# Kernel tuning notes

Measured on AMD Instinct MI355X. Metric: run time of the kernel, lower is better.

## Reference

```python
import jax, jax.numpy as jnp
import numpy as np
import math

CH_IN, MID, PS, DSTATE = 64, 128, 1024, 16
DTRANK = math.ceil(PS / 16)  # 64
B, H, W = 4, 256, 256


def conv2d(x, w, b=None, stride=1, pad=0, groups=1):
    out = jax.lax.conv_general_dilated(
        x, w, (stride, stride), [(pad, pad), (pad, pad)],
        feature_group_count=groups, dimension_numbers=('NCHW', 'OIHW', 'NCHW'))
    return out if b is None else out + b[None, :, None, None]


def groupnorm(x, g, b, ngroups=2, eps=1e-5):
    bb, c, hh, ww = x.shape
    xr = x.reshape(bb, ngroups, c // ngroups, hh, ww)
    mu = xr.mean(axis=(2, 3, 4), keepdims=True)
    var = xr.var(axis=(2, 3, 4), keepdims=True)
    xn = ((xr - mu) * jax.lax.rsqrt(var + eps)).reshape(bb, c, hh, ww)
    return xn * g[None, :, None, None] + b[None, :, None, None]


def silu(x):
    return x * jax.nn.sigmoid(x)


def selective_scan(u, delta, A, Bm, Cm, D):
    # u, delta: (b, l, d); A: (d, n); Bm, Cm: (b, l, n); D: (d,)
    dA = jnp.exp(jnp.einsum('bld,dn->bldn', delta, A))          # (b,l,d,n)
    dBu = (delta * u)[..., None] * Bm[:, :, None, :]             # (b,l,d,n)
    bsz, l, d = u.shape
    n = A.shape[1]

    def step(carry, inp):
        dA_i, dBu_i, C_i = inp                                   # (b,d,n),(b,d,n),(b,n)
        carry = dA_i * carry + dBu_i
        y = jnp.einsum('bdn,bn->bd', carry, C_i)
        return carry, y

    x0 = jnp.zeros((bsz, d, n), dtype=u.dtype)
    _, ys = jax.lax.scan(step, x0, (dA.transpose(1, 0, 2, 3), dBu.transpose(1, 0, 2, 3), Cm.transpose(1, 0, 2)))
    y = ys.transpose(1, 0, 2)                                    # (b,l,d)
    return y + u * D


def mamba_block(x, inproj_w, conv_w, conv_b, xproj_w, dtp_w, dtp_b, alog, dd):
    xr = conv2d(x, inproj_w, None, 1, 1, MID // 2)               # (b, 2*MID, h, w)
    xs, res = jnp.split(xr, 2, axis=1)
    xs = silu(conv2d(xs, conv_w, conv_b, 1, 0, MID // 2))
    b, c, h, w = xs.shape
    u = xs.reshape(b, c, h * w)                                  # (b, l=c, d=h*w)
    A = -jnp.exp(alog.astype(jnp.float32))                       # (d, n)
    x_dbl = jnp.einsum('bld,kd->blk', u, xproj_w)
    delta, Bm, Cm = jnp.split(x_dbl, [DTRANK, DTRANK + DSTATE], axis=-1)
    delta = jax.nn.softplus(jnp.einsum('blr,dr->bld', delta, dtp_w) + dtp_b)
    y = selective_scan(u, delta, A, Bm, Cm, dd.astype(jnp.float32))
    y = y.reshape(b, c, h, w)
    return y * silu(res)


def forward(x, w_in, b_in,
            gn0_g, gn0_b, inproj0_w, conv0_w, conv0_b, xproj0_w, dtp0_w, dtp0_b, alog0, dd0,
            gn1_g, gn1_b, inproj1_w, conv1_w, conv1_b, xproj1_w, dtp1_w, dtp1_b, alog1, dd1,
            w_out, b_out):
    h = conv2d(x, w_in, b_in, 8, 0, CH_IN // 2)                  # (B, MID, H/8, W/8)
    h = mamba_block(groupnorm(h, gn0_g, gn0_b), inproj0_w, conv0_w, conv0_b, xproj0_w, dtp0_w, dtp0_b, alog0, dd0) + h
    h = mamba_block(groupnorm(h, gn1_g, gn1_b), inproj1_w, conv1_w, conv1_b, xproj1_w, dtp1_w, dtp1_b, alog1, dd1) + h
    out = conv2d(h, w_out, b_out, 1, 0, CH_IN // 2)
    out = jax.image.resize(out, (out.shape[0], out.shape[1], out.shape[2] * 8, out.shape[3] * 8), method='bilinear')
    return out


def setup_inputs():
    key = jax.random.key(0)
    ks = jax.random.split(key, 16)
    def rn(k, shp, s=0.05):
        return s * jax.random.normal(k, shp, jnp.float32)
    alog = jnp.log(jnp.broadcast_to(jnp.arange(1, DSTATE + 1, dtype=jnp.float32), (PS, DSTATE)))
    inp = {
        'x': jax.random.normal(ks[0], (B, CH_IN, H, W), jnp.float32),
        'w_in': rn(ks[1], (MID, 2, 8, 8)), 'b_in': jnp.zeros((MID,), jnp.float32),
        'gn0_g': jnp.ones((MID,), jnp.float32), 'gn0_b': jnp.zeros((MID,), jnp.float32),
        'inproj0_w': rn(ks[2], (2 * MID, 2, 3, 3)),
        'conv0_w': rn(ks[3], (MID, 2, 1, 1)), 'conv0_b': jnp.zeros((MID,), jnp.float32),
        'xproj0_w': rn(ks[4], (DTRANK + 2 * DSTATE, PS), 0.02),
        'dtp0_w': rn(ks[5], (PS, DTRANK), 0.02), 'dtp0_b': rn(ks[6], (PS,), 0.02),
        'alog0': alog, 'dd0': jnp.ones((PS,), jnp.float32),
        'gn1_g': jnp.ones((MID,), jnp.float32), 'gn1_b': jnp.zeros((MID,), jnp.float32),
        'inproj1_w': rn(ks[7], (2 * MID, 2, 3, 3)),
        'conv1_w': rn(ks[8], (MID, 2, 1, 1)), 'conv1_b': jnp.zeros((MID,), jnp.float32),
        'xproj1_w': rn(ks[9], (DTRANK + 2 * DSTATE, PS), 0.02),
        'dtp1_w': rn(ks[10], (PS, DTRANK), 0.02), 'dtp1_b': rn(ks[11], (PS,), 0.02),
        'alog1': alog, 'dd1': jnp.ones((PS,), jnp.float32),
        'w_out': rn(ks[12], (MID, MID // (CH_IN // 2), 1, 1)), 'b_out': jnp.zeros((MID,), jnp.float32),
    }
    return inp


def reference(x, w_in, b_in,
              gn0_g, gn0_b, inproj0_w, conv0_w, conv0_b, xproj0_w, dtp0_w, dtp0_b, alog0, dd0,
              gn1_g, gn1_b, inproj1_w, conv1_w, conv1_b, xproj1_w, dtp1_w, dtp1_b, alog1, dd1,
              w_out, b_out):
    return forward(x, w_in, b_in,
                   gn0_g, gn0_b, inproj0_w, conv0_w, conv0_b, xproj0_w, dtp0_w, dtp0_b, alog0, dd0,
                   gn1_g, gn1_b, inproj1_w, conv1_w, conv1_b, xproj1_w, dtp1_w, dtp1_b, alog1, dd1,
                   w_out, b_out)
```

## Files before the change

kernel.cpp:

```cpp
#include <hip/hip_runtime.h>
#include <hip/hip_bf16.h>

#define BN 4
#define MID 128
#define P 1024
#define PS 1024
#define DSTATE 16
#define DTRANK 64
#define XD 96
#define HOUT 256

typedef __hip_bfloat16 bf16;

__device__ __forceinline__ float b2f(bf16 v) { return __bfloat162float(v); }
__device__ __forceinline__ float dload(const void* p, int i, bool isbf) {
  return isbf ? b2f(((const bf16*)p)[i]) : ((const float*)p)[i];
}
__device__ __forceinline__ float bfl(unsigned u) {
  union { unsigned i; float f; } c; c.i = u << 16; return c.f;
}
__device__ __forceinline__ float bfh(unsigned u) {
  union { unsigned i; float f; } c; c.i = u & 0xffff0000u; return c.f;
}

#define NPARAM 24
#define TOTAL_PARAMS 392192
#define CONV_PER_BLOCK 766
struct PtrPack { const void* p[NPARAM]; };

__device__ __forceinline__ void find_tensor(int dst, int& tt, int& off) {
  const int offs[NPARAM + 1] = {0,16384,16512,16640,16768,21376,21632,21760,120064,185600,
                                186624,203008,204032,204160,204288,208896,209152,209280,
                                307584,373120,374144,390528,391552,392064,392192};
  int t = 0, base = 0;
#pragma unroll
  for (int q = 1; q < NPARAM; ++q) {
    if (dst >= offs[q]) { t = q; base = offs[q]; }
  }
  tt = t; off = dst - base;
}

__global__ __launch_bounds__(256) void conv_in_kernel(
    const void* __restrict__ x, const unsigned* __restrict__ alog_raw,
    PtrPack pk, float* __restrict__ pp, float* __restrict__ h,
    float2* __restrict__ partA) {
  bool isbf = (alog_raw[0] != 0u);
  int blk = blockIdx.x, t = threadIdx.x;

  for (int i = t; i < CONV_PER_BLOCK; i += 256) {
    int dst = blk * CONV_PER_BLOCK + i;
    int tt, off;
    find_tensor(dst, tt, off);
    int src = off;
    if (tt == 7 || tt == 17) {
      int j = off & 3, q = off >> 2;
      int k = q % 96, d4 = q / 96;
      src = k * 1024 + d4 * 4 + j;
    } else if (tt == 8 || tt == 18) {
      src = (off & 1023) * 64 + (off >> 10);
    }
    pp[dst] = dload(pk.p[tt], src, isbf);
  }

  __shared__ float wlds[512];
  __shared__ float blds[4];
  __shared__ float ls[8];
  int tid = blk * 256 + t;
  int p = tid & 1023; int g = (tid >> 10) & 31; int b = tid >> 15;
  for (int q = t; q < 512; q += 256) {
    int i = q >> 8, kh = (q >> 5) & 7, j = (q >> 3) & 3, kw = q & 7;
    wlds[q] = dload(pk.p[0], (g * 4 + j) * 128 + i * 64 + kh * 8 + kw, isbf);
  }
  if (t < 4) blds[t] = dload(pk.p[1], g * 4 + t, isbf);
  __syncthreads();

  int oy = p >> 5, ox = p & 31;
  float acc0 = blds[0], acc1 = blds[1], acc2 = blds[2], acc3 = blds[3];
  if (isbf) {
    const uint4* xp = (const uint4*)x;
    size_t base = ((size_t)b * 64 + g * 2) * 8192;
    for (int i = 0; i < 2; ++i) {
      size_t cb = base + (size_t)i * 8192 + (size_t)oy * 256 + ox;
#pragma unroll
      for (int kh = 0; kh < 8; ++kh) {
        uint4 v = xp[cb + kh * 32];
        float xv[8] = {bfl(v.x),bfh(v.x),bfl(v.y),bfh(v.y),bfl(v.z),bfh(v.z),bfl(v.w),bfh(v.w)};
        const float* wk = &wlds[(i * 8 + kh) * 32];
#pragma unroll
        for (int kw = 0; kw < 8; ++kw) {
          float xvv = xv[kw];
          acc0 += xvv * wk[kw];
          acc1 += xvv * wk[8 + kw];
          acc2 += xvv * wk[16 + kw];
          acc3 += xvv * wk[24 + kw];
        }
      }
    }
  } else {
    const float4* xf = (const float4*)x;
    size_t base = ((size_t)b * 64 + g * 2) * 16384;
    for (int i = 0; i < 2; ++i) {
      size_t cb = base + (size_t)i * 16384 + (size_t)oy * 512 + ox * 2;
#pragma unroll
      for (int kh = 0; kh < 8; ++kh) {
        float4 v0 = xf[cb + kh * 64];
        float4 v1 = xf[cb + kh * 64 + 1];
        float xv[8] = {v0.x,v0.y,v0.z,v0.w,v1.x,v1.y,v1.z,v1.w};
        const float* wk = &wlds[(i * 8 + kh) * 32];
#pragma unroll
        for (int kw = 0; kw < 8; ++kw) {
          float xvv = xv[kw];
          acc0 += xvv * wk[kw];
          acc1 += xvv * wk[8 + kw];
          acc2 += xvv * wk[16 + kw];
          acc3 += xvv * wk[24 + kw];
        }
      }
    }
  }
  size_t ob = ((size_t)b * 128 + g * 4) * 1024 + p;
  h[ob] = acc0; h[ob + 1024] = acc1; h[ob + 2048] = acc2; h[ob + 3072] = acc3;

  float s  = acc0 + acc1 + acc2 + acc3;
  float s2 = acc0*acc0 + acc1*acc1 + acc2*acc2 + acc3*acc3;
#pragma unroll
  for (int off = 32; off > 0; off >>= 1) { s += __shfl_xor(s, off); s2 += __shfl_xor(s2, off); }
  int wid = t >> 6;
  if ((t & 63) == 0) { ls[wid * 2] = s; ls[wid * 2 + 1] = s2; }
  __syncthreads();
  if (t == 0)
    partA[blk] = make_float2(ls[0] + ls[2] + ls[4] + ls[6], ls[1] + ls[3] + ls[5] + ls[7]);
}

__global__ __launch_bounds__(256) void fused_u_kernel(
    const float* __restrict__ h, const float2* __restrict__ partial, int perB, int cnt,
    const float* __restrict__ gng, const float* __restrict__ gnb,
    const float* __restrict__ iw, const float* __restrict__ cw,
    const float* __restrict__ cb, float* __restrict__ u) {
  int blk = blockIdx.x;
  int h2 = blk & 1, g3 = (blk >> 1) & 31, b = blk >> 6;
  int ic0 = g3 * 2;
  __shared__ float tile[2][34][36];
  __shared__ float sred[2];
  if (threadIdx.x < 64) {
    float s = 0.f, s2 = 0.f;
    int base = b * perB;
    for (int i = threadIdx.x; i < cnt; i += 64) { float2 v = partial[base + i]; s += v.x; s2 += v.y; }
#pragma unroll
    for (int off = 32; off > 0; off >>= 1) { s += __shfl_xor(s, off); s2 += __shfl_xor(s2, off); }
    if (threadIdx.x == 0) { sred[0] = s; sred[1] = s2; }
  }
  for (int t = threadIdx.x; t < 2448; t += 256) ((float*)tile)[t] = 0.f;
  __syncthreads();
  float mu = sred[0] * (1.f / 65536.f);
  float var = sred[1] * (1.f / 65536.f) - mu * mu;
  float rs = rsqrtf(var + 1e-5f);
  float a0 = rs * gng[ic0],     o0 = gnb[ic0]     - mu * a0;
  float a1 = rs * gng[ic0 + 1], o1 = gnb[ic0 + 1] - mu * a1;
  const float* h0 = h + ((size_t)b * MID + ic0) * P;
  for (int t = threadIdx.x; t < 2048; t += 256) {
    int ch = t >> 10, px = t & 1023, y = px >> 5, xx = px & 31;
    float v = h0[ch * P + px];
    tile[ch][y + 1][xx + 1] = ch ? (v * a1 + o1) : (v * a0 + o0);
  }
  __syncthreads();
  const float* w0 = iw + (size_t)(4 * g3) * 18;
#pragma unroll
  for (int q = 0; q < 2; ++q) {
    int px = h2 * 512 + q * 256 + threadIdx.x;
    int y = px >> 5, xx = px & 31;
    float nb0[9], nb1[9];
#pragma unroll
    for (int ky = 0; ky < 3; ++ky)
#pragma unroll
      for (int kx = 0; kx < 3; ++kx) {
        nb0[ky * 3 + kx] = tile[0][y + ky][xx + kx];
        nb1[ky * 3 + kx] = tile[1][y + ky][xx + kx];
      }
    float xsv[4];
#pragma unroll
    for (int s4 = 0; s4 < 4; ++s4) {
      const float* wr = w0 + s4 * 18;
      float acc = 0.f;
#pragma unroll
      for (int k = 0; k < 9; ++k) acc += nb0[k] * wr[k] + nb1[k] * wr[9 + k];
      xsv[s4] = acc;
    }
#pragma unroll
    for (int j = 0; j < 4; ++j) {
      int c = 4 * g3 + j;
      int e4 = (j >> 1) * 2;
      float acc = cb[c] + cw[2 * c] * xsv[e4] + cw[2 * c + 1] * xsv[e4 + 1];
      u[((size_t)b * MID + c) * P + px] = acc / (1.f + __expf(-acc));
    }
  }
}

__global__ __launch_bounds__(256) void xdbl_delta_kernel(
    const float* __restrict__ u, const float* __restrict__ xwp,
    const float* __restrict__ dwt, const float* __restrict__ db,
    float* __restrict__ dlt_t, float* __restrict__ u_t, float* __restrict__ bct) {
  int bl = blockIdx.x;
  int b = bl >> 7, l = bl & 127;
  int t = threadIdx.x;
  __shared__ float4 us[256];
  __shared__ float4 accs[96];
  __shared__ float xds[64];
  const float4* up = (const float4*)(u + (size_t)bl * P);
  us[t] = up[t];
  __syncthreads();

  float4 acc = make_float4(0.f, 0.f, 0.f, 0.f);
  if (t < 192) {
    int s = (t >= 96) ? 1 : 0, k = t - s * 96;
    const float4* wp = (const float4*)xwp;
#pragma unroll 4
    for (int i = 0; i < 128; ++i) {
      int d4 = 2 * i + s;
      float4 w4 = wp[d4 * 96 + k];
      float4 u4 = us[d4];
      acc.x += u4.x * w4.x; acc.y += u4.y * w4.y; acc.z += u4.z * w4.z; acc.w += u4.w * w4.w;
    }
    if (s) accs[k] = acc;
  } else {
    float* ubase = u_t + ((size_t)b * 1024) * 128 + l;
    const float* usf = (const float*)us;
    for (int i = t - 192; i < 1024; i += 64) ubase[(size_t)i * 128] = usf[i];
  }
  __syncthreads();
  if (t < 96) {
    float4 o = accs[t];
    acc.x += o.x; acc.y += o.y; acc.z += o.z; acc.w += o.w;
    float v = (acc.x + acc.y) + (acc.z + acc.w);
    if (t < 64) xds[t] = v;
    else bct[((size_t)b * 32 + (t - 64)) * 128 + l] = v;
  }
  __syncthreads();

  float a0 = db[t], a1 = db[t + 256], a2 = db[t + 512], a3 = db[t + 768];
#pragma unroll 8
  for (int r = 0; r < 64; ++r) {
    float xr = xds[r];
    const float* wr = dwt + r * 1024 + t;
    a0 += xr * wr[0];
    a1 += xr * wr[256];
    a2 += xr * wr[512];
    a3 += xr * wr[768];
  }
  float* dbase = dlt_t + ((size_t)b * 1024) * 128 + l;
  float vals[4] = {a0, a1, a2, a3};
#pragma unroll
  for (int j = 0; j < 4; ++j) {
    float a = vals[j];
    float sp = fmaxf(a, 0.f) + log1pf(__expf(-fabsf(a)));
    dbase[(size_t)(t + 256 * j) * 128] = sp;
  }
}

__global__ __launch_bounds__(256) void scan_kernel(
    const float* __restrict__ u_t, const float* __restrict__ dlt_t,
    const float* __restrict__ bct, const float* __restrict__ alog,
    const float* __restrict__ dd, float* __restrict__ y_t) {
  int tid = blockIdx.x * 256 + threadIdx.x;
  int n = tid & 15; int d = (tid >> 4) & 1023; int b = tid >> 14;
  float A = -__expf(alog[d * DSTATE + n]);
  float D = dd[d];
  const float4* ut = (const float4*)(u_t   + ((size_t)b * 1024 + d) * 128);
  const float4* dt = (const float4*)(dlt_t + ((size_t)b * 1024 + d) * 128);
  const float4* Bt = (const float4*)(bct + ((size_t)b * 32 + n) * 128);
  const float4* Ct = (const float4*)(bct + ((size_t)b * 32 + 16 + n) * 128);
  float4* yp = (float4*)(y_t + ((size_t)b * 1024 + d) * 128);
  float state = 0.f;
#pragma unroll 2
  for (int lc = 0; lc < 32; ++lc) {
    float4 dl4 = dt[lc], u4 = ut[lc], B4 = Bt[lc], C4 = Ct[lc];
    float4 yo;
#define SSTEP(c) { float dA = __expf(dl4.c * A); state = dA * state + dl4.c * u4.c * B4.c; \
    float yv = state * C4.c; yv += __shfl_xor(yv, 1, 16); yv += __shfl_xor(yv, 2, 16); \
    yv += __shfl_xor(yv, 4, 16); yv += __shfl_xor(yv, 8, 16); yo.c = yv + u4.c * D; }
    SSTEP(x) SSTEP(y) SSTEP(z) SSTEP(w)
#undef SSTEP
    if (n == 0) yp[lc] = yo;
  }
}

__global__ __launch_bounds__(256) void merge_res_kernel(
    const float* __restrict__ hin, const float2* __restrict__ partial, int perB, int cnt,
    const float* __restrict__ gng, const float* __restrict__ gnb,
    const float* __restrict__ iw, const float* __restrict__ y_t,
    float* __restrict__ hout, float2* __restrict__ part_out) {
  int blk = blockIdx.x;
  int h2 = blk & 1, gq = (blk >> 1) & 31, b = blk >> 6;
  int g = 32 + gq;
  int ic0 = g * 2;
  __shared__ float tile[2][34][36];
  __shared__ float sred[2];
  __shared__ float ls[8];
  if (threadIdx.x < 64) {
    float s = 0.f, s2 = 0.f;
    int base = b * perB + cnt;
    for (int i = threadIdx.x; i < cnt; i += 64) { float2 v = partial[base + i]; s += v.x; s2 += v.y; }
#pragma unroll
    for (int off = 32; off > 0; off >>= 1) { s += __shfl_xor(s, off); s2 += __shfl_xor(s2, off); }
    if (threadIdx.x == 0) { sred[0] = s; sred[1] = s2; }
  }
  for (int t = threadIdx.x; t < 2448; t += 256) ((float*)tile)[t] = 0.f;
  __syncthreads();
  float mu = sred[0] * (1.f / 65536.f);
  float var = sred[1] * (1.f / 65536.f) - mu * mu;
  float rs = rsqrtf(var + 1e-5f);
  float a0 = rs * gng[ic0],     o0 = gnb[ic0]     - mu * a0;
  float a1 = rs * gng[ic0 + 1], o1 = gnb[ic0 + 1] - mu * a1;
  const float* h0 = hin + ((size_t)b * MID + ic0) * P;
  for (int t = threadIdx.x; t < 2048; t += 256) {
    int ch = t >> 10, px = t & 1023, y = px >> 5, xx = px & 31;
    float v = h0[ch * P + px];
    tile[ch][y + 1][xx + 1] = ch ? (v * a1 + o1) : (v * a0 + o0);
  }
  __syncthreads();
  const float* w0 = iw + (size_t)(4 * g) * 18;
  float sacc = 0.f, s2acc = 0.f;
#pragma unroll
  for (int q = 0; q < 2; ++q) {
    int px = h2 * 512 + q * 256 + threadIdx.x;
    int y = px >> 5, xx = px & 31;
    float nb0[9], nb1[9];
#pragma unroll
    for (int ky = 0; ky < 3; ++ky)
#pragma unroll
      for (int kx = 0; kx < 3; ++kx) {
        nb0[ky * 3 + kx] = tile[0][y + ky][xx + kx];
        nb1[ky * 3 + kx] = tile[1][y + ky][xx + kx];
      }
    float4 yv4 = *(const float4*)(y_t + ((size_t)b * 1024 + px) * 128 + gq * 4);
    float yv[4] = {yv4.x, yv4.y, yv4.z, yv4.w};
#pragma unroll
    for (int j = 0; j < 4; ++j) {
      const float* wr = w0 + j * 18;
      float res = 0.f;
#pragma unroll
      for (int k = 0; k < 9; ++k) res += nb0[k] * wr[k] + nb1[k] * wr[9 + k];
      int c = 4 * gq + j;
      size_t oi = ((size_t)b * MID + c) * P + px;
      float s = res / (1.f + __expf(-res));
      float val = yv[j] * s + hin[oi];
      hout[oi] = val;
      sacc += val; s2acc += val * val;
    }
  }
  if (part_out) {
#pragma unroll
    for (int off = 32; off > 0; off >>= 1) { sacc += __shfl_xor(sacc, off); s2acc += __shfl_xor(s2acc, off); }
    int wid = threadIdx.x >> 6;
    if ((threadIdx.x & 63) == 0) { ls[wid * 2] = sacc; ls[wid * 2 + 1] = s2acc; }
    __syncthreads();
    if (threadIdx.x == 0)
      part_out[blk] = make_float2(ls[0] + ls[2] + ls[4] + ls[6], ls[1] + ls[3] + ls[5] + ls[7]);
  }
}

__global__ __launch_bounds__(256) void out_kernel(
    const float* __restrict__ h, const float* __restrict__ w, const float* __restrict__ bias,
    const unsigned* __restrict__ alog_raw, void* __restrict__ out) {
  int bc = blockIdx.x;
  int c = bc & 127, b = bc >> 7;
  int t = threadIdx.x;
  __shared__ float cop[1024];
  __shared__ float txs[256];
  __shared__ int x0s[256], x1s[256];
  {
    float cx = ((float)t + 0.5f) * 0.125f - 0.5f;
    int ix0 = (int)floorf(cx);
    txs[t] = cx - (float)ix0;
    x0s[t] = max(ix0, 0);
    x1s[t] = min(ix0 + 1, 31);
  }
  const float* hp = h + ((size_t)b * MID + (c & ~3)) * P;
  float w0 = w[c * 4], w1 = w[c * 4 + 1], w2 = w[c * 4 + 2], w3 = w[c * 4 + 3];
  float bo = bias[c];
  {
    const float4* h4 = (const float4*)hp;
    float4 v0 = h4[t], v1 = h4[256 + t], v2 = h4[512 + t], v3 = h4[768 + t];
    float4 a;
    a.x = bo + w0 * v0.x + w1 * v1.x + w2 * v2.x + w3 * v3.x;
    a.y = bo + w0 * v0.y + w1 * v1.y + w2 * v2.y + w3 * v3.y;
    a.z = bo + w0 * v0.z + w1 * v1.z + w2 * v2.z + w3 * v3.z;
    a.w = bo + w0 * v0.w + w1 * v1.w + w2 * v2.w + w3 * v3.w;
    ((float4*)cop)[t] = a;
  }
  __syncthreads();
  bool isbf = (alog_raw[0] != 0u);
  size_t obase = (size_t)bc * 16384;
  for (int gidx = t; gidx < 16384; gidx += 256) {
    int ox4 = gidx & 63, oy = gidx >> 6;
    float ty = txs[oy]; int y0 = x0s[oy], y1 = x1s[oy];
    const float* r0 = cop + y0 * 32;
    const float* r1 = cop + y1 * 32;
    float v[4];
#pragma unroll
    for (int j = 0; j < 4; ++j) {
      int ox = ox4 * 4 + j;
      float tx = txs[ox]; int xx0 = x0s[ox], xx1 = x1s[ox];
      float v00 = r0[xx0], v01 = r0[xx1], v10 = r1[xx0], v11 = r1[xx1];
      v[j] = (1.f - ty) * ((1.f - tx) * v00 + tx * v01) + ty * ((1.f - tx) * v10 + tx * v11);
    }
    if (isbf) {
      ushort4 s;
      s.x = __hip_bfloat16_raw(__float2bfloat16(v[0])).x;
      s.y = __hip_bfloat16_raw(__float2bfloat16(v[1])).x;
      s.z = __hip_bfloat16_raw(__float2bfloat16(v[2])).x;
      s.w = __hip_bfloat16_raw(__float2bfloat16(v[3])).x;
      ((ushort4*)out)[obase + gidx] = s;
    } else {
      ((float4*)out)[obase + gidx] = make_float4(v[0], v[1], v[2], v[3]);
    }
  }
}

extern "C" void kernel_launch(void* const* d_in, const int* in_sizes, int n_in,
                              void* d_out, int out_size, void* d_ws, size_t ws_size,
                              hipStream_t stream) {
  const void* x = d_in[0];
  const unsigned* alog_raw = (const unsigned*)d_in[11];

  PtrPack pk;
  for (int i = 0; i < NPARAM; ++i) pk.p[i] = d_in[i + 1];

  float* ws = (float*)d_ws;
  float* pp    = ws;
  float* h0    = pp + TOTAL_PARAMS;
  float* h1    = h0 + 524288;
  float* u     = h1 + 524288;
  float* u_t   = u + 524288;
  float* dlt_t = u_t + 524288;
  float* y_t   = dlt_t + 524288;
  float* bct   = y_t + 524288;
  float* partA = bct + 16384;
  float* partB = partA + 1024;

  const float* w_out = pp + 391552;
  const float* b_out = pp + 392064;
  const float* gn_g[2], *gn_b[2], *inproj_w[2], *conv_w[2], *conv_b[2],
             *xproj_w[2], *dtp_w[2], *dtp_b[2], *alog_f[2], *dd_f[2];
  for (int k = 0; k < 2; ++k) {
    const float* base = pp + 16512 + (size_t)k * 187520;
    gn_g[k] = base + 0;       gn_b[k] = base + 128;
    inproj_w[k] = base + 256; conv_w[k] = base + 4864;
    conv_b[k] = base + 5120;  xproj_w[k] = base + 5248;
    dtp_w[k] = base + 103552; dtp_b[k] = base + 169088;
    alog_f[k] = base + 170112; dd_f[k] = base + 186496;
  }

  conv_in_kernel<<<512, 256, 0, stream>>>(x, alog_raw, pk, pp, h0, (float2*)partA);

  float* hbuf[2] = { h0, h1 };
  const float2* partIn = (const float2*)partA;
  int perB = 128, cnt = 64;
  for (int blk = 0; blk < 2; ++blk) {
    float* hin  = hbuf[blk & 1];
    float* hout = hbuf[(blk + 1) & 1];
    fused_u_kernel<<<256, 256, 0, stream>>>(hin, partIn, perB, cnt, gn_g[blk], gn_b[blk],
                                            inproj_w[blk], conv_w[blk], conv_b[blk], u);
    xdbl_delta_kernel<<<512, 256, 0, stream>>>(u, xproj_w[blk], dtp_w[blk], dtp_b[blk],
                                               dlt_t, u_t, bct);
    scan_kernel<<<256, 256, 0, stream>>>(u_t, dlt_t, bct, alog_f[blk], dd_f[blk], y_t);
    merge_res_kernel<<<256, 256, 0, stream>>>(hin, partIn, perB, cnt, gn_g[blk], gn_b[blk],
                                              inproj_w[blk], y_t, hout,
                                              blk == 0 ? (float2*)partB : nullptr);
    partIn = (const float2*)partB; perB = 64; cnt = 32;
  }

  out_kernel<<<512, 256, 0, stream>>>(h0, w_out, b_out, alog_raw, d_out);
}
```

Measured before the change: 355.6 us.

## Fuse all stages into one persistent kernel with atomic grid barriers

Replaces the nine separate kernel launches with a single persistent kernel of 512 blocks that runs every stage and separates them with software grid barriers built on atomic counters, which are zeroed by a memset before launch. Fused_u and merge now use 512 blocks handling 256 pixels each instead of 256 blocks handling 512, and the scan stage idles half the blocks. The goal is to remove launch gaps and tail effects between stages. In exchange it depends on all 512 blocks being co-resident, since the barrier wait gives up after a bounded spin, and it adds barrier spin overhead and possible occupancy limits from the shared-memory union.

```diff
diff --git a/kernel.cpp b/kernel.cpp
--- a/kernel.cpp
+++ b/kernel.cpp
@@ -26,7 +26,30 @@
 #define NPARAM 24
 #define TOTAL_PARAMS 392192
 #define CONV_PER_BLOCK 766
+#define NBLK 512u
 struct PtrPack { const void* p[NPARAM]; };
+
+__device__ __forceinline__ void gsync(unsigned* slot) {
+  __syncthreads();
+  if (threadIdx.x == 0) {
+    __threadfence();
+    __hip_atomic_fetch_add(slot, 1u, __ATOMIC_RELAXED, __HIP_MEMORY_SCOPE_AGENT);
+    unsigned guard = 0;
+    while (__hip_atomic_load(slot, __ATOMIC_RELAXED, __HIP_MEMORY_SCOPE_AGENT) < NBLK) {
+      __builtin_amdgcn_s_sleep(2);
+      if (++guard > (1u << 24)) break;
+    }
+    __threadfence();
+  }
+  __syncthreads();
+}
+
+union Smem {
+  struct { float wlds[512]; float blds[4]; float ls[8]; } s0;
+  struct { float tile[2][34][36]; float sred[2]; float ls[8]; } s1;
+  struct { float4 us[256]; float4 accs[96]; float xds[64]; } s2;
+  struct { float cop[1024]; float txs[256]; int x0s[256]; int x1s[256]; } s5;
+};
 
 __device__ __forceinline__ void find_tensor(int dst, int& tt, int& off) {
   const int offs[NPARAM + 1] = {0,16384,16512,16640,16768,21376,21632,21760,120064,185600,
@@ -40,11 +63,9 @@
   tt = t; off = dst - base;
 }
 
-__global__ __launch_bounds__(256) void conv_in_kernel(
-    const void* __restrict__ x, const unsigned* __restrict__ alog_raw,
-    PtrPack pk, float* __restrict__ pp, float* __restrict__ h,
-    float2* __restrict__ partA) {
-  bool isbf = (alog_raw[0] != 0u);
+__device__ __forceinline__ void stage_conv_in(const void* __restrict__ x, bool isbf,
+    const PtrPack& pk, float* __restrict__ pp, float* __restrict__ h,
+    float2* __restrict__ partA, Smem& sm) {
   int blk = blockIdx.x, t = threadIdx.x;
 
   for (int i = t; i < CONV_PER_BLOCK; i += 256) {
@@ -62,20 +83,17 @@
     pp[dst] = dload(pk.p[tt], src, isbf);
   }
 
-  __shared__ float wlds[512];
-  __shared__ float blds[4];
-  __shared__ float ls[8];
   int tid = blk * 256 + t;
   int p = tid & 1023; int g = (tid >> 10) & 31; int b = tid >> 15;
   for (int q = t; q < 512; q += 256) {
     int i = q >> 8, kh = (q >> 5) & 7, j = (q >> 3) & 3, kw = q & 7;
-    wlds[q] = dload(pk.p[0], (g * 4 + j) * 128 + i * 64 + kh * 8 + kw, isbf);
-  }
-  if (t < 4) blds[t] = dload(pk.p[1], g * 4 + t, isbf);
+    sm.s0.wlds[q] = dload(pk.p[0], (g * 4 + j) * 128 + i * 64 + kh * 8 + kw, isbf);
+  }
+  if (t < 4) sm.s0.blds[t] = dload(pk.p[1], g * 4 + t, isbf);
   __syncthreads();
 
   int oy = p >> 5, ox = p & 31;
-  float acc0 = blds[0], acc1 = blds[1], acc2 = blds[2], acc3 = blds[3];
+  float acc0 = sm.s0.blds[0], acc1 = sm.s0.blds[1], acc2 = sm.s0.blds[2], acc3 = sm.s0.blds[3];
   if (isbf) {
     const uint4* xp = (const uint4*)x;
     size_t base = ((size_t)b * 64 + g * 2) * 8192;
@@ -85,7 +103,7 @@
       for (int kh = 0; kh < 8; ++kh) {
         uint4 v = xp[cb + kh * 32];
         float xv[8] = {bfl(v.x),bfh(v.x),bfl(v.y),bfh(v.y),bfl(v.z),bfh(v.z),bfl(v.w),bfh(v.w)};
-        const float* wk = &wlds[(i * 8 + kh) * 32];
+        const float* wk = &sm.s0.wlds[(i * 8 + kh) * 32];
 #pragma unroll
         for (int kw = 0; kw < 8; ++kw) {
           float xvv = xv[kw];
@@ -106,7 +124,7 @@
         float4 v0 = xf[cb + kh * 64];
         float4 v1 = xf[cb + kh * 64 + 1];
         float xv[8] = {v0.x,v0.y,v0.z,v0.w,v1.x,v1.y,v1.z,v1.w};
-        const float* wk = &wlds[(i * 8 + kh) * 32];
+        const float* wk = &sm.s0.wlds[(i * 8 + kh) * 32];
 #pragma unroll
         for (int kw = 0; kw < 8; ++kw) {
           float xvv = xv[kw];
@@ -126,34 +144,32 @@
 #pragma unroll
   for (int off = 32; off > 0; off >>= 1) { s += __shfl_xor(s, off); s2 += __shfl_xor(s2, off); }
   int wid = t >> 6;
-  if ((t & 63) == 0) { ls[wid * 2] = s; ls[wid * 2 + 1] = s2; }
+  if ((t & 63) == 0) { sm.s0.ls[wid * 2] = s; sm.s0.ls[wid * 2 + 1] = s2; }
   __syncthreads();
   if (t == 0)
-    partA[blk] = make_float2(ls[0] + ls[2] + ls[4] + ls[6], ls[1] + ls[3] + ls[5] + ls[7]);
-}
-
-__global__ __launch_bounds__(256) void fused_u_kernel(
-    const float* __restrict__ h, const float2* __restrict__ partial, int perB, int cnt,
-    const float* __restrict__ gng, const float* __restrict__ gnb,
-    const float* __restrict__ iw, const float* __restrict__ cw,
-    const float* __restrict__ cb, float* __restrict__ u) {
-  int blk = blockIdx.x;
-  int h2 = blk & 1, g3 = (blk >> 1) & 31, b = blk >> 6;
+    partA[blk] = make_float2(sm.s0.ls[0] + sm.s0.ls[2] + sm.s0.ls[4] + sm.s0.ls[6],
+                             sm.s0.ls[1] + sm.s0.ls[3] + sm.s0.ls[5] + sm.s0.ls[7]);
+}
+
+__device__ __forceinline__ void stage_fused_u(const float* __restrict__ h,
+    const float2* __restrict__ partial, const float* __restrict__ gng,
+    const float* __restrict__ gnb, const float* __restrict__ iw,
+    const float* __restrict__ cw, const float* __restrict__ cb,
+    float* __restrict__ u, Smem& sm) {
+  int pb = blockIdx.x;
+  int h4 = pb & 3, g3 = (pb >> 2) & 31, b = pb >> 7;
   int ic0 = g3 * 2;
-  __shared__ float tile[2][34][36];
-  __shared__ float sred[2];
   if (threadIdx.x < 64) {
-    float s = 0.f, s2 = 0.f;
-    int base = b * perB;
-    for (int i = threadIdx.x; i < cnt; i += 64) { float2 v = partial[base + i]; s += v.x; s2 += v.y; }
+    float2 v = partial[b * 128 + threadIdx.x];
+    float s = v.x, s2 = v.y;
 #pragma unroll
     for (int off = 32; off > 0; off >>= 1) { s += __shfl_xor(s, off); s2 += __shfl_xor(s2, off); }
-    if (threadIdx.x == 0) { sred[0] = s; sred[1] = s2; }
-  }
-  for (int t = threadIdx.x; t < 2448; t += 256) ((float*)tile)[t] = 0.f;
-  __syncthreads();
-  float mu = sred[0] * (1.f / 65536.f);
-  float var = sred[1] * (1.f / 65536.f) - mu * mu;
+    if (threadIdx.x == 0) { sm.s1.sred[0] = s; sm.s1.sred[1] = s2; }
+  }
+  for (int t = threadIdx.x; t < 2448; t += 256) ((float*)sm.s1.tile)[t] = 0.f;
+  __syncthreads();
+  float mu = sm.s1.sred[0] * (1.f / 65536.f);
+  float var = sm.s1.sred[1] * (1.f / 65536.f) - mu * mu;
   float rs = rsqrtf(var + 1e-5f);
   float a0 = rs * gng[ic0],     o0 = gnb[ic0]     - mu * a0;
   float a1 = rs * gng[ic0 + 1], o1 = gnb[ic0 + 1] - mu * a1;
@@ -161,53 +177,47 @@
   for (int t = threadIdx.x; t < 2048; t += 256) {
     int ch = t >> 10, px = t & 1023, y = px >> 5, xx = px & 31;
     float v = h0[ch * P + px];
-    tile[ch][y + 1][xx + 1] = ch ? (v * a1 + o1) : (v * a0 + o0);
+    sm.s1.tile[ch][y + 1][xx + 1] = ch ? (v * a1 + o1) : (v * a0 + o0);
   }
   __syncthreads();
   const float* w0 = iw + (size_t)(4 * g3) * 18;
-#pragma unroll
-  for (int q = 0; q < 2; ++q) {
-    int px = h2 * 512 + q * 256 + threadIdx.x;
-    int y = px >> 5, xx = px & 31;
-    float nb0[9], nb1[9];
-#pragma unroll
-    for (int ky = 0; ky < 3; ++ky)
-#pragma unroll
-      for (int kx = 0; kx < 3; ++kx) {
-        nb0[ky * 3 + kx] = tile[0][y + ky][xx + kx];
-        nb1[ky * 3 + kx] = tile[1][y + ky][xx + kx];
-      }
-    float xsv[4];
-#pragma unroll
-    for (int s4 = 0; s4 < 4; ++s4) {
-      const float* wr = w0 + s4 * 18;
-      float acc = 0.f;
-#pragma unroll
-      for (int k = 0; k < 9; ++k) acc += nb0[k] * wr[k] + nb1[k] * wr[9 + k];
-      xsv[s4] = acc;
-    }
-#pragma unroll
-    for (int j = 0; j < 4; ++j) {
-      int c = 4 * g3 + j;
-      int e4 = (j >> 1) * 2;
-      float acc = cb[c] + cw[2 * c] * xsv[e4] + cw[2 * c + 1] * xsv[e4 + 1];
-      u[((size_t)b * MID + c) * P + px] = acc / (1.f + __expf(-acc));
-    }
-  }
-}
-
-__global__ __launch_bounds__(256) void xdbl_delta_kernel(
-    const float* __restrict__ u, const float* __restrict__ xwp,
-    const float* __restrict__ dwt, const float* __restrict__ db,
-    float* __restrict__ dlt_t, float* __restrict__ u_t, float* __restrict__ bct) {
+  int px = h4 * 256 + threadIdx.x;
+  int y = px >> 5, xx = px & 31;
+  float nb0[9], nb1[9];
+#pragma unroll
+  for (int ky = 0; ky < 3; ++ky)
+#pragma unroll
+    for (int kx = 0; kx < 3; ++kx) {
+      nb0[ky * 3 + kx] = sm.s1.tile[0][y + ky][xx + kx];
+      nb1[ky * 3 + kx] = sm.s1.tile[1][y + ky][xx + kx];
+    }
+  float xsv[4];
+#pragma unroll
+  for (int s4 = 0; s4 < 4; ++s4) {
+    const float* wr = w0 + s4 * 18;
+    float acc = 0.f;
+#pragma unroll
+    for (int k = 0; k < 9; ++k) acc += nb0[k] * wr[k] + nb1[k] * wr[9 + k];
+    xsv[s4] = acc;
+  }
+#pragma unroll
+  for (int j = 0; j < 4; ++j) {
+    int c = 4 * g3 + j;
+    int e4 = (j >> 1) * 2;
+    float acc = cb[c] + cw[2 * c] * xsv[e4] + cw[2 * c + 1] * xsv[e4 + 1];
+    u[((size_t)b * MID + c) * P + px] = acc / (1.f + __expf(-acc));
+  }
+}
+
+__device__ __forceinline__ void stage_xdbl(const float* __restrict__ u,
+    const float* __restrict__ xwp, const float* __restrict__ dwt,
+    const float* __restrict__ db, float* __restrict__ dlt_t,
+    float* __restrict__ u_t, float* __restrict__ bct, Smem& sm) {
   int bl = blockIdx.x;
   int b = bl >> 7, l = bl & 127;
   int t = threadIdx.x;
-  __shared__ float4 us[256];
-  __shared__ float4 accs[96];
-  __shared__ float xds[64];
   const float4* up = (const float4*)(u + (size_t)bl * P);
-  us[t] = up[t];
+  sm.s2.us[t] = up[t];
   __syncthreads();
 
   float4 acc = make_float4(0.f, 0.f, 0.f, 0.f);
@@ -218,21 +228,21 @@
     for (int i = 0; i < 128; ++i) {
       int d4 = 2 * i + s;
       float4 w4 = wp[d4 * 96 + k];
-      float4 u4 = us[d4];
+      float4 u4 = sm.s2.us[d4];
       acc.x += u4.x * w4.x; acc.y += u4.y * w4.y; acc.z += u4.z * w4.z; acc.w += u4.w * w4.w;
     }
-    if (s) accs[k] = acc;
+    if (s) sm.s2.accs[k] = acc;
   } else {
     float* ubase = u_t + ((size_t)b * 1024) * 128 + l;
-    const float* usf = (const float*)us;
+    const float* usf = (const float*)sm.s2.us;
     for (int i = t - 192; i < 1024; i += 64) ubase[(size_t)i * 128] = usf[i];
   }
   __syncthreads();
   if (t < 96) {
-    float4 o = accs[t];
+    float4 o = sm.s2.accs[t];
     acc.x += o.x; acc.y += o.y; acc.z += o.z; acc.w += o.w;
     float v = (acc.x + acc.y) + (acc.z + acc.w);
-    if (t < 64) xds[t] = v;
+    if (t < 64) sm.s2.xds[t] = v;
     else bct[((size_t)b * 32 + (t - 64)) * 128 + l] = v;
   }
   __syncthreads();
@@ -240,7 +250,7 @@
   float a0 = db[t], a1 = db[t + 256], a2 = db[t + 512], a3 = db[t + 768];
 #pragma unroll 8
   for (int r = 0; r < 64; ++r) {
-    float xr = xds[r];
+    float xr = sm.s2.xds[r];
     const float* wr = dwt + r * 1024 + t;
     a0 += xr * wr[0];
     a1 += xr * wr[256];
@@ -257,10 +267,11 @@
   }
 }
 
-__global__ __launch_bounds__(256) void scan_kernel(
-    const float* __restrict__ u_t, const float* __restrict__ dlt_t,
-    const float* __restrict__ bct, const float* __restrict__ alog,
-    const float* __restrict__ dd, float* __restrict__ y_t) {
+__device__ __forceinline__ void stage_scan(const float* __restrict__ u_t,
+    const float* __restrict__ dlt_t, const float* __restrict__ bct,
+    const float* __restrict__ alog, const float* __restrict__ dd,
+    float* __restrict__ y_t) {
+  if (blockIdx.x >= 256) return;
   int tid = blockIdx.x * 256 + threadIdx.x;
   int n = tid & 15; int d = (tid >> 4) & 1023; int b = tid >> 14;
   float A = -__expf(alog[d * DSTATE + n]);
@@ -284,30 +295,26 @@
   }
 }
 
-__global__ __launch_bounds__(256) void merge_res_kernel(
-    const float* __restrict__ hin, const float2* __restrict__ partial, int perB, int cnt,
-    const float* __restrict__ gng, const float* __restrict__ gnb,
-    const float* __restrict__ iw, const float* __restrict__ y_t,
-    float* __restrict__ hout, float2* __restrict__ part_out) {
-  int blk = blockIdx.x;
-  int h2 = blk & 1, gq = (blk >> 1) & 31, b = blk >> 6;
+__device__ __forceinline__ void stage_merge(const float* __restrict__ hin,
+    const float2* __restrict__ partial, const float* __restrict__ gng,
+    const float* __restrict__ gnb, const float* __restrict__ iw,
+    const float* __restrict__ y_t, float* __restrict__ hout,
+    float2* __restrict__ part_out, Smem& sm) {
+  int pb = blockIdx.x;
+  int h4 = pb & 3, gq = (pb >> 2) & 31, b = pb >> 7;
   int g = 32 + gq;
   int ic0 = g * 2;
-  __shared__ float tile[2][34][36];
-  __shared__ float sred[2];
-  __shared__ float ls[8];
   if (threadIdx.x < 64) {
-    float s = 0.f, s2 = 0.f;
-    int base = b * perB + cnt;
-    for (int i = threadIdx.x; i < cnt; i += 64) { float2 v = partial[base + i]; s += v.x; s2 += v.y; }
+    float2 v = partial[b * 128 + 64 + threadIdx.x];
+    float s = v.x, s2 = v.y;
 #pragma unroll
     for (int off = 32; off > 0; off >>= 1) { s += __shfl_xor(s, off); s2 += __shfl_xor(s2, off); }
-    if (threadIdx.x == 0) { sred[0] = s; sred[1] = s2; }
-  }
-  for (int t = threadIdx.x; t < 2448; t += 256) ((float*)tile)[t] = 0.f;
-  __syncthreads();
-  float mu = sred[0] * (1.f / 65536.f);
-  float var = sred[1] * (1.f / 65536.f) - mu * mu;
+    if (threadIdx.x == 0) { sm.s1.sred[0] = s; sm.s1.sred[1] = s2; }
+  }
+  for (int t = threadIdx.x; t < 2448; t += 256) ((float*)sm.s1.tile)[t] = 0.f;
+  __syncthreads();
+  float mu = sm.s1.sred[0] * (1.f / 65536.f);
+  float var = sm.s1.sred[1] * (1.f / 65536.f) - mu * mu;
   float rs = rsqrtf(var + 1e-5f);
   float a0 = rs * gng[ic0],     o0 = gnb[ic0]     - mu * a0;
   float a1 = rs * gng[ic0 + 1], o1 = gnb[ic0 + 1] - mu * a1;
@@ -315,65 +322,60 @@
   for (int t = threadIdx.x; t < 2048; t += 256) {
     int ch = t >> 10, px = t & 1023, y = px >> 5, xx = px & 31;
     float v = h0[ch * P + px];
-    tile[ch][y + 1][xx + 1] = ch ? (v * a1 + o1) : (v * a0 + o0);
+    sm.s1.tile[ch][y + 1][xx + 1] = ch ? (v * a1 + o1) : (v * a0 + o0);
   }
   __syncthreads();
   const float* w0 = iw + (size_t)(4 * g) * 18;
   float sacc = 0.f, s2acc = 0.f;
-#pragma unroll
-  for (int q = 0; q < 2; ++q) {
-    int px = h2 * 512 + q * 256 + threadIdx.x;
-    int y = px >> 5, xx = px & 31;
-    float nb0[9], nb1[9];
-#pragma unroll
-    for (int ky = 0; ky < 3; ++ky)
-#pragma unroll
-      for (int kx = 0; kx < 3; ++kx) {
-        nb0[ky * 3 + kx] = tile[0][y + ky][xx + kx];
-        nb1[ky * 3 + kx] = tile[1][y + ky][xx + kx];
-      }
-    float4 yv4 = *(const float4*)(y_t + ((size_t)b * 1024 + px) * 128 + gq * 4);
-    float yv[4] = {yv4.x, yv4.y, yv4.z, yv4.w};
-#pragma unroll
-    for (int j = 0; j < 4; ++j) {
-      const float* wr = w0 + j * 18;
-      float res = 0.f;
-#pragma unroll
-      for (int k = 0; k < 9; ++k) res += nb0[k] * wr[k] + nb1[k] * wr[9 + k];
-      int c = 4 * gq + j;
-      size_t oi = ((size_t)b * MID + c) * P + px;
-      float s = res / (1.f + __expf(-res));
-      float val = yv[j] * s + hin[oi];
-      hout[oi] = val;
-      sacc += val; s2acc += val * val;
-    }
+  int px = h4 * 256 + threadIdx.x;
+  int y = px >> 5, xx = px & 31;
+  float nb0[9], nb1[9];
+#pragma unroll
+  for (int ky = 0; ky < 3; ++ky)
+#pragma unroll
+    for (int kx = 0; kx < 3; ++kx) {
+      nb0[ky * 3 + kx] = sm.s1.tile[0][y + ky][xx + kx];
+      nb1[ky * 3 + kx] = sm.s1.tile[1][y + ky][xx + kx];
+    }
+  float4 yv4 = *(const float4*)(y_t + ((size_t)b * 1024 + px) * 128 + gq * 4);
+  float yv[4] = {yv4.x, yv4.y, yv4.z, yv4.w};
+#pragma unroll
+  for (int j = 0; j < 4; ++j) {
+    const float* wr = w0 + j * 18;
+    float res = 0.f;
+#pragma unroll
+    for (int k = 0; k < 9; ++k) res += nb0[k] * wr[k] + nb1[k] * wr[9 + k];
+    int c = 4 * gq + j;
+    size_t oi = ((size_t)b * MID + c) * P + px;
+    float s = res / (1.f + __expf(-res));
+    float val = yv[j] * s + hin[oi];
+    hout[oi] = val;
+    sacc += val; s2acc += val * val;
   }
   if (part_out) {
 #pragma unroll
     for (int off = 32; off > 0; off >>= 1) { sacc += __shfl_xor(sacc, off); s2acc += __shfl_xor(s2acc, off); }
     int wid = threadIdx.x >> 6;
-    if ((threadIdx.x & 63) == 0) { ls[wid * 2] = sacc; ls[wid * 2 + 1] = s2acc; }
+    if ((threadIdx.x & 63) == 0) { sm.s1.ls[wid * 2] = sacc; sm.s1.ls[wid * 2 + 1] = s2acc; }
     __syncthreads();
     if (threadIdx.x == 0)
-      part_out[blk] = make_float2(ls[0] + ls[2] + ls[4] + ls[6], ls[1] + ls[3] + ls[5] + ls[7]);
-  }
-}
-
-__global__ __launch_bounds__(256) void out_kernel(
-    const float* __restrict__ h, const float* __restrict__ w, const float* __restrict__ bias,
-    const unsigned* __restrict__ alog_raw, void* __restrict__ out) {
+      part_out[pb] = make_float2(sm.s1.ls[0] + sm.s1.ls[2] + sm.s1.ls[4] + sm.s1.ls[6],
+                                 sm.s1.ls[1] + sm.s1.ls[3] + sm.s1.ls[5] + sm.s1.ls[7]);
+  }
+}
+
+__device__ __forceinline__ void stage_out(const float* __restrict__ h,
+    const float* __restrict__ w, const float* __restrict__ bias, bool isbf,
+    void* __restrict__ out, Smem& sm) {
   int bc = blockIdx.x;
   int c = bc & 127, b = bc >> 7;
   int t = threadIdx.x;
-  __shared__ float cop[1024];
-  __shared__ float txs[256];
-  __shared__ int x0s[256], x1s[256];
   {
     float cx = ((float)t + 0.5f) * 0.125f - 0.5f;
     int ix0 = (int)floorf(cx);
-    txs[t] = cx - (float)ix0;
-    x0s[t] = max(ix0, 0);
-    x1s[t] = min(ix0 + 1, 31);
+    sm.s5.txs[t] = cx - (float)ix0;
+    sm.s5.x0s[t] = max(ix0, 0);
+    sm.s5.x1s[t] = min(ix0 + 1, 31);
   }
   const float* hp = h + ((size_t)b * MID + (c & ~3)) * P;
   float w0 = w[c * 4], w1 = w[c * 4 + 1], w2 = w[c * 4 + 2], w3 = w[c * 4 + 3];
@@ -386,21 +388,20 @@
     a.y = bo + w0 * v0.y + w1 * v1.y + w2 * v2.y + w3 * v3.y;
     a.z = bo + w0 * v0.z + w1 * v1.z + w2 * v2.z + w3 * v3.z;
     a.w = bo + w0 * v0.w + w1 * v1.w + w2 * v2.w + w3 * v3.w;
-    ((float4*)cop)[t] = a;
-  }
-  __syncthreads();
-  bool isbf = (alog_raw[0] != 0u);
+    ((float4*)sm.s5.cop)[t] = a;
+  }
+  __syncthreads();
   size_t obase = (size_t)bc * 16384;
   for (int gidx = t; gidx < 16384; gidx += 256) {
     int ox4 = gidx & 63, oy = gidx >> 6;
-    float ty = txs[oy]; int y0 = x0s[oy], y1 = x1s[oy];
-    const float* r0 = cop + y0 * 32;
-    const float* r1 = cop + y1 * 32;
+    float ty = sm.s5.txs[oy]; int y0 = sm.s5.x0s[oy], y1 = sm.s5.x1s[oy];
+    const float* r0 = sm.s5.cop + y0 * 32;
+    const float* r1 = sm.s5.cop + y1 * 32;
     float v[4];
 #pragma unroll
     for (int j = 0; j < 4; ++j) {
       int ox = ox4 * 4 + j;
-      float tx = txs[ox]; int xx0 = x0s[ox], xx1 = x1s[ox];
+      float tx = sm.s5.txs[ox]; int xx0 = sm.s5.x0s[ox], xx1 = sm.s5.x1s[ox];
       float v00 = r0[xx0], v01 = r0[xx1], v10 = r1[xx0], v11 = r1[xx1];
       v[j] = (1.f - ty) * ((1.f - tx) * v00 + tx * v01) + ty * ((1.f - tx) * v10 + tx * v11);
     }
@@ -417,6 +418,51 @@
   }
 }
 
+__global__ __launch_bounds__(256, 2) void mega_kernel(
+    const void* __restrict__ x, const unsigned* __restrict__ alog_raw,
+    PtrPack pk, float* __restrict__ ws, void* __restrict__ out) {
+  __shared__ Smem sm;
+  bool isbf = (alog_raw[0] != 0u);
+
+  float* pp    = ws;
+  float* h0    = ws + 392192;
+  float* h1    = ws + 916480;
+  float* u     = ws + 1440768;
+  float* u_t   = ws + 1965056;
+  float* dlt_t = ws + 2489344;
+  float* y_t   = ws + 3013632;
+  float* bct   = ws + 3537920;
+  float2* partA = (float2*)(ws + 3554304);
+  float2* partB = (float2*)(ws + 3555328);
+  unsigned* bar = (unsigned*)(ws + 3556352);
+  int bs = 0;
+
+  stage_conv_in(x, isbf, pk, pp, h0, partA, sm);
+  gsync(&bar[bs++]);
+
+  for (int blk = 0; blk < 2; ++blk) {
+    const float* base = pp + 16512 + blk * 187520;
+    const float* gng = base, *gnb = base + 128, *iw = base + 256;
+    const float* cw = base + 4864, *cb = base + 5120;
+    const float* xwp = base + 5248, *dwt = base + 103552, *db = base + 169088;
+    const float* alog = base + 170112, *dd = base + 186496;
+    float* hin  = blk ? h1 : h0;
+    float* hout = blk ? h0 : h1;
+    const float2* pIn = blk ? partB : partA;
+
+    stage_fused_u(hin, pIn, gng, gnb, iw, cw, cb, u, sm);
+    gsync(&bar[bs++]);
+    stage_xdbl(u, xwp, dwt, db, dlt_t, u_t, bct, sm);
+    gsync(&bar[bs++]);
+    stage_scan(u_t, dlt_t, bct, alog, dd, y_t);
+    gsync(&bar[bs++]);
+    stage_merge(hin, pIn, gng, gnb, iw, y_t, hout, blk == 0 ? partB : nullptr, sm);
+    gsync(&bar[bs++]);
+  }
+
+  stage_out(h0, pp + 391552, pp + 392064, isbf, out, sm);
+}
+
 extern "C" void kernel_launch(void* const* d_in, const int* in_sizes, int n_in,
                               void* d_out, int out_size, void* d_ws, size_t ws_size,
                               hipStream_t stream) {
@@ -427,48 +473,8 @@
   for (int i = 0; i < NPARAM; ++i) pk.p[i] = d_in[i + 1];
 
   float* ws = (float*)d_ws;
-  float* pp    = ws;
-  float* h0    = pp + TOTAL_PARAMS;
-  float* h1    = h0 + 524288;
-  float* u     = h1 + 524288;
-  float* u_t   = u + 524288;
-  float* dlt_t = u_t + 524288;
-  float* y_t   = dlt_t + 524288;
-  float* bct   = y_t + 524288;
-  float* partA = bct + 16384;
-  float* partB = partA + 1024;
-
-  const float* w_out = pp + 391552;
-  const float* b_out = pp + 392064;
-  const float* gn_g[2], *gn_b[2], *inproj_w[2], *conv_w[2], *conv_b[2],
-             *xproj_w[2], *dtp_w[2], *dtp_b[2], *alog_f[2], *dd_f[2];
-  for (int k = 0; k < 2; ++k) {
-    const float* base = pp + 16512 + (size_t)k * 187520;
-    gn_g[k] = base + 0;       gn_b[k] = base + 128;
-    inproj_w[k] = base + 256; conv_w[k] = base + 4864;
-    conv_b[k] = base + 5120;  xproj_w[k] = base + 5248;
-    dtp_w[k] = base + 103552; dtp_b[k] = base + 169088;
-    alog_f[k] = base + 170112; dd_f[k] = base + 186496;
-  }
-
-  conv_in_kernel<<<512, 256, 0, stream>>>(x, alog_raw, pk, pp, h0, (float2*)partA);
-
-  float* hbuf[2] = { h0, h1 };
-  const float2* partIn = (const float2*)partA;
-  int perB = 128, cnt = 64;
-  for (int blk = 0; blk < 2; ++blk) {
-    float* hin  = hbuf[blk & 1];
-    float* hout = hbuf[(blk + 1) & 1];
-    fused_u_kernel<<<256, 256, 0, stream>>>(hin, partIn, perB, cnt, gn_g[blk], gn_b[blk],
-                                            inproj_w[blk], conv_w[blk], conv_b[blk], u);
-    xdbl_delta_kernel<<<512, 256, 0, stream>>>(u, xproj_w[blk], dtp_w[blk], dtp_b[blk],
-                                               dlt_t, u_t, bct);
-    scan_kernel<<<256, 256, 0, stream>>>(u_t, dlt_t, bct, alog_f[blk], dd_f[blk], y_t);
-    merge_res_kernel<<<256, 256, 0, stream>>>(hin, partIn, perB, cnt, gn_g[blk], gn_b[blk],
-                                              inproj_w[blk], y_t, hout,
-                                              blk == 0 ? (float2*)partB : nullptr);
-    partIn = (const float2*)partB; perB = 64; cnt = 32;
-  }
-
-  out_kernel<<<512, 256, 0, stream>>>(h0, w_out, b_out, alog_raw, d_out);
-}
+
+  hipMemsetAsync((char*)d_ws + (size_t)3556352 * 4, 0, 64, stream);
+
+  mega_kernel<<<512, 256, 0, stream>>>(x, alog_raw, pk, ws, d_out);
+}
```

New measurement: 860.5 us. 2.42x slower.
